# Performance work log

Measured on AMD Instinct MI355X. Metric: run time of the kernel, lower is better.

## Reference

```python
import jax, jax.numpy as jnp
import numpy as np

N = 20000   # nodes
E = 320000  # directed edges (before self-loops)
D = 64      # input_dim
H = 10      # GAT heads
HD = H * D  # 640
NEG_SLOPE = 0.2


def setup_inputs() -> dict:
    key = jax.random.key(0)
    ks = jax.random.split(key, 10)
    return {
        "x": jax.random.normal(ks[0], (N, D), jnp.float32),
        "W_gat": jax.random.normal(ks[1], (D, HD), jnp.float32) / np.sqrt(D).astype(np.float32),
        "att_src": jax.random.normal(ks[2], (H, D), jnp.float32) / np.sqrt(D).astype(np.float32),
        "att_dst": jax.random.normal(ks[3], (H, D), jnp.float32) / np.sqrt(D).astype(np.float32),
        "b_gat": jnp.zeros((HD,), jnp.float32),
        "W_gcn": jax.random.normal(ks[4], (HD, HD), jnp.float32) / np.sqrt(HD).astype(np.float32),
        "b_gcn": jnp.zeros((HD,), jnp.float32),
        "W1": jax.random.normal(ks[5], (2 * HD, 1500), jnp.float32) / np.sqrt(2 * HD).astype(np.float32),
        "b1": jnp.zeros((1500,), jnp.float32),
        "W2": jax.random.normal(ks[6], (1500, 10), jnp.float32) / np.sqrt(1500).astype(np.float32),
        "b2": jnp.zeros((10,), jnp.float32),
        "edge_index": jax.random.randint(ks[7], (2, E), 0, N, dtype=jnp.int64),
    }


def _forward(x, W_gat, att_src, att_dst, b_gat, W_gcn, b_gcn, W1, b1, W2, b2, edge_index):
    n = x.shape[0]
    # add self-loops (PyG default for both GATConv and GCNConv)
    loop = jnp.arange(n, dtype=edge_index.dtype)
    ei = jnp.concatenate([edge_index, jnp.stack([loop, loop])], axis=1)
    src, dst = ei[0], ei[1]

    # ---- GATConv(D -> D, heads=H, concat) ----
    xl = (x @ W_gat).reshape(n, H, D)                      # [N,H,D]
    a_src = jnp.einsum('nhd,hd->nh', xl, att_src)          # [N,H]
    a_dst = jnp.einsum('nhd,hd->nh', xl, att_dst)          # [N,H]
    alpha = jax.nn.leaky_relu(a_src[src] + a_dst[dst], NEG_SLOPE)  # [E',H]
    m = jax.ops.segment_max(alpha, dst, num_segments=n)    # segment softmax over incoming edges
    ex = jnp.exp(alpha - m[dst])
    den = jax.ops.segment_sum(ex, dst, num_segments=n)
    w = ex / (den[dst] + 1e-16)                            # [E',H]
    msg = xl[src] * w[:, :, None]                          # [E',H,D]
    x1 = jax.ops.segment_sum(msg, dst, num_segments=n).reshape(n, HD) + b_gat
    x1 = jax.nn.relu(x1)

    # ---- GCNConv(HD -> HD), symmetric norm with self-loops ----
    deg = jax.ops.segment_sum(jnp.ones(ei.shape[1], x.dtype), dst, num_segments=n)
    dinv = jnp.where(deg > 0, jax.lax.rsqrt(deg), 0.0)
    norm = dinv[src] * dinv[dst]                           # [E']
    xw = x1 @ W_gcn                                        # [N,HD]
    x2 = jax.ops.segment_sum(xw[src] * norm[:, None], dst, num_segments=n) + b_gcn
    x2 = jax.nn.relu(x2)

    # ---- global max/mean pool (batch=None -> single graph) + MLP head ----
    pooled = jnp.concatenate([x2.max(axis=0, keepdims=True),
                              x2.mean(axis=0, keepdims=True)], axis=1)  # [1, 2*HD]
    h = jax.nn.relu(pooled @ W1 + b1)
    # dropout is identity in eval mode
    return h @ W2 + b2                                     # [1, 10]


def reference(x, W_gat, att_src, att_dst, b_gat, W_gcn, b_gcn, W1, b1, W2, b2, edge_index):
    return _forward(x, W_gat, att_src, att_dst, b_gat, W_gcn, b_gcn, W1, b1, W2, b2, edge_index)
```

## Files before the change

kernel.cpp:

```cpp
#include <hip/hip_runtime.h>
#include <hip/hip_bf16.h>
#include <math.h>

#define NN 20000
#define DD 64
#define HH 10
#define HDIM 640
#define NEG 0.2f
#define H1 1500
#define ASTRIDE 12
#define BKK 128

typedef _Float16 half8 __attribute__((ext_vector_type(8)));
typedef _Float16 half4v __attribute__((ext_vector_type(4)));
typedef float f32x4 __attribute__((ext_vector_type(4)));

__global__ __launch_bounds__(256) void k_cvtB(const float* __restrict__ Wgcn,
                                              const float* __restrict__ Wg,
                                              _Float16* __restrict__ Wbt,
                                              _Float16* __restrict__ WgT)
{
    __shared__ float t[32][33];
    const int bx = blockIdx.x;
    int by = blockIdx.y;
    const float* W; _Float16* WT; int rows, cols;
    if (by < 20) { W = Wgcn; WT = Wbt; rows = HDIM; cols = HDIM; }
    else         { W = Wg;   WT = WgT; rows = DD;   cols = HDIM; by -= 20; }
    const int lx = threadIdx.x & 31, ly = threadIdx.x >> 5;
    #pragma unroll
    for (int i = ly; i < 32; i += 8)
        t[i][lx] = W[(size_t)(by * 32 + i) * cols + bx * 32 + lx];
    __syncthreads();
    #pragma unroll
    for (int j = ly; j < 32; j += 8)
        WT[(size_t)(bx * 32 + j) * rows + by * 32 + lx] = (_Float16)t[lx][j];
}

__global__ __launch_bounds__(256) void k_gemm1(
    const float* __restrict__ x, const _Float16* __restrict__ WgT,
    const float* __restrict__ att_s, const float* __restrict__ att_d,
    _Float16* __restrict__ xl, float* __restrict__ a_src, float* __restrict__ a_dst)
{
    __shared__ _Float16 As[128][72];
    __shared__ _Float16 Bs[64][72];
    const int tid = threadIdx.x;
    const int m0 = blockIdx.x * 128;
    const int h  = blockIdx.y;
    const int n0 = h * 64;

    {
        const int row = tid >> 1, ch = (tid & 1) * 32;
        const int gr = m0 + row;
        if (gr < NN) {
            const float* xp = &x[(size_t)gr * DD + ch];
            #pragma unroll
            for (int i = 0; i < 8; ++i) {
                const float4 v = *(const float4*)&xp[i * 4];
                half4v o = {(_Float16)v.x, (_Float16)v.y, (_Float16)v.z, (_Float16)v.w};
                *(half4v*)&As[row][ch + i * 4] = o;
            }
        } else {
            const half8 z = {0, 0, 0, 0, 0, 0, 0, 0};
            #pragma unroll
            for (int i = 0; i < 4; ++i) *(half8*)&As[row][ch + i * 8] = z;
        }
    }
    {
        const int row = tid >> 2, part = (tid & 3) * 16;
        const _Float16* wp = &WgT[(size_t)(n0 + row) * DD + part];
        *(half8*)&Bs[row][part]     = *(const half8*)&wp[0];
        *(half8*)&Bs[row][part + 8] = *(const half8*)&wp[8];
    }
    __syncthreads();

    const int lane = tid & 63, wave = tid >> 6;
    const int l15 = lane & 15, quad = lane >> 4;
    f32x4 acc[2][4];
    #pragma unroll
    for (int r = 0; r < 2; ++r)
        #pragma unroll
        for (int c = 0; c < 4; ++c) acc[r][c] = (f32x4){0.f, 0.f, 0.f, 0.f};

    #pragma unroll
    for (int ks = 0; ks < 2; ++ks) {
        const half8 a0 = *(const half8*)&As[wave * 32 + l15][ks * 32 + quad * 8];
        const half8 a1 = *(const half8*)&As[wave * 32 + 16 + l15][ks * 32 + quad * 8];
        #pragma unroll
        for (int c = 0; c < 4; ++c) {
            const half8 b = *(const half8*)&Bs[c * 16 + l15][ks * 32 + quad * 8];
            acc[0][c] = __builtin_amdgcn_mfma_f32_16x16x32_f16(a0, b, acc[0][c], 0, 0, 0);
            acc[1][c] = __builtin_amdgcn_mfma_f32_16x16x32_f16(a1, b, acc[1][c], 0, 0, 0);
        }
    }

    float asv[4], adv[4];
    #pragma unroll
    for (int c = 0; c < 4; ++c) {
        asv[c] = att_s[h * DD + c * 16 + l15];
        adv[c] = att_d[h * DD + c * 16 + l15];
    }
    #pragma unroll
    for (int r = 0; r < 2; ++r) {
        float ps[4] = {0.f, 0.f, 0.f, 0.f}, pd[4] = {0.f, 0.f, 0.f, 0.f};
        #pragma unroll
        for (int c = 0; c < 4; ++c)
            #pragma unroll
            for (int g = 0; g < 4; ++g) {
                ps[g] = fmaf(acc[r][c][g], asv[c], ps[g]);
                pd[g] = fmaf(acc[r][c][g], adv[c], pd[g]);
            }
        #pragma unroll
        for (int m = 1; m <= 8; m <<= 1)
            #pragma unroll
            for (int g = 0; g < 4; ++g) {
                ps[g] += __shfl_xor(ps[g], m);
                pd[g] += __shfl_xor(pd[g], m);
            }
        #pragma unroll
        for (int c = 0; c < 4; ++c)
            #pragma unroll
            for (int g = 0; g < 4; ++g) {
                const int row = m0 + wave * 32 + r * 16 + quad * 4 + g;
                if (row < NN)
                    xl[(size_t)row * HDIM + n0 + c * 16 + l15] = (_Float16)acc[r][c][g];
            }
        if (l15 == 0)
            #pragma unroll
            for (int g = 0; g < 4; ++g) {
                const int row = m0 + wave * 32 + r * 16 + quad * 4 + g;
                if (row < NN) {
                    a_src[(size_t)row * ASTRIDE + h] = ps[g];
                    a_dst[(size_t)row * ASTRIDE + h] = pd[g];
                }
            }
    }
}

__global__ void k_count(const int* __restrict__ ei, int E, int* __restrict__ cnt)
{
    const int e = blockIdx.x * blockDim.x + threadIdx.x;
    if (e >= E + NN) return;
    const int d = (e < E) ? ei[E + e] : (e - E);
    atomicAdd(&cnt[d], 1);
}

__global__ __launch_bounds__(1024) void k_scan(const int* __restrict__ cnt,
                                               int* __restrict__ rowptr,
                                               float* __restrict__ dinv)
{
    __shared__ int sh[1024];
    const int t = threadIdx.x;
    const int CH = 20;
    const int base = t * CH;
    int loc[CH];
    int s = 0;
    #pragma unroll
    for (int i = 0; i < CH; ++i) {
        const int idx = base + i;
        const int c = (idx < NN) ? cnt[idx] : 0;
        loc[i] = s; s += c;
    }
    sh[t] = s; __syncthreads();
    for (int off = 1; off < 1024; off <<= 1) {
        const int v = (t >= off) ? sh[t - off] : 0;
        __syncthreads();
        sh[t] += v;
        __syncthreads();
    }
    const int prev = (t == 0) ? 0 : sh[t - 1];
    #pragma unroll
    for (int i = 0; i < CH; ++i) {
        const int idx = base + i;
        if (idx < NN) {
            rowptr[idx] = prev + loc[i];
            dinv[idx]   = rsqrtf((float)cnt[idx]);
        }
    }
    if (t == 1023) rowptr[NN] = sh[1023];
}

__global__ void k_fill(const int* __restrict__ ei, int E,
                       const int* __restrict__ rowptr,
                       int* __restrict__ cursor, int* __restrict__ csr,
                       const float* __restrict__ dinv, float* __restrict__ wn,
                       const float* __restrict__ aS, const float* __restrict__ aD,
                       float* __restrict__ wgatT)
{
    const int EP = E + NN;
    const int e = blockIdx.x * blockDim.x + threadIdx.x;
    if (e >= EP) return;
    int s, d;
    if (e < E) { s = ei[e]; d = ei[E + e]; } else { s = d = e - E; }
    const int pos = atomicAdd(&cursor[d], 1);
    const int idx = rowptr[d] + pos;
    csr[idx] = s;
    wn[idx]  = dinv[s] * dinv[d];

    const f32x4 s0 = *(const f32x4*)&aS[(size_t)s * ASTRIDE];
    const f32x4 s1 = *(const f32x4*)&aS[(size_t)s * ASTRIDE + 4];
    const float2 s2 = *(const float2*)&aS[(size_t)s * ASTRIDE + 8];
    const f32x4 d0 = *(const f32x4*)&aD[(size_t)d * ASTRIDE];
    const f32x4 d1 = *(const f32x4*)&aD[(size_t)d * ASTRIDE + 4];
    const float2 d2 = *(const float2*)&aD[(size_t)d * ASTRIDE + 8];
    const float av[10] = {s0.x + d0.x, s0.y + d0.y, s0.z + d0.z, s0.w + d0.w,
                          s1.x + d1.x, s1.y + d1.y, s1.z + d1.z, s1.w + d1.w,
                          s2.x + d2.x, s2.y + d2.y};
    #pragma unroll
    for (int h = 0; h < 10; ++h) {
        float a = av[h];
        a = (a >= 0.f) ? a : NEG * a;
        wgatT[(size_t)h * EP + idx] = __expf(a);
    }
}

__device__ __forceinline__ bool slice_map3(int bid, int& s, int& m)
{
    const int r = bid & 7, k = bid >> 3;
    if (k < 625) { s = r; m = k; return true; }
    s = 8 + (r >> 2);
    m = (r & 3) * 157 + (k - 625);
    return m < 625;
}

__global__ __launch_bounds__(256) void k_gat_gather3(
    const int* __restrict__ rowptr, const int* __restrict__ csr,
    const float* __restrict__ wgatT, const _Float16* __restrict__ xl,
    const float* __restrict__ b_gat, _Float16* __restrict__ x1, int EP)
{
    int s, m;
    if (!slice_map3(blockIdx.x, s, m)) return;
    const int wave = threadIdx.x >> 6, lane = threadIdx.x & 63;
    const int g = lane >> 3, l = lane & 7;
    const int n = m * 32 + wave * 8 + g;
    const int col = s * 64 + l * 8;
    const float* __restrict__ wp = wgatT + (size_t)s * EP;
    const _Float16* __restrict__ xc = xl + col;

    float acc[8];
    #pragma unroll
    for (int i = 0; i < 8; ++i) acc[i] = 0.f;
    float ws = 0.f;

    const int j0 = rowptr[n], j1 = rowptr[n + 1];
    int j = j0;
    for (; j + 3 < j1; j += 4) {
        const int sA = csr[j], sB = csr[j + 1], sC = csr[j + 2], sD = csr[j + 3];
        const float wA = wp[j], wB = wp[j + 1], wC = wp[j + 2], wD = wp[j + 3];
        ws += wA + wB + wC + wD;
        const half8 vA = *(const half8*)&xc[(size_t)sA * HDIM];
        const half8 vB = *(const half8*)&xc[(size_t)sB * HDIM];
        const half8 vC = *(const half8*)&xc[(size_t)sC * HDIM];
        const half8 vD = *(const half8*)&xc[(size_t)sD * HDIM];
        #pragma unroll
        for (int i = 0; i < 8; ++i) {
            acc[i] = fmaf(wA, (float)vA[i], acc[i]);
            acc[i] = fmaf(wB, (float)vB[i], acc[i]);
            acc[i] = fmaf(wC, (float)vC[i], acc[i]);
            acc[i] = fmaf(wD, (float)vD[i], acc[i]);
        }
    }
    for (; j < j1; ++j) {
        const int sA = csr[j];
        const float wA = wp[j];
        ws += wA;
        const half8 vA = *(const half8*)&xc[(size_t)sA * HDIM];
        #pragma unroll
        for (int i = 0; i < 8; ++i) acc[i] = fmaf(wA, (float)vA[i], acc[i]);
    }

    const float rr = 1.f / (ws + 1e-16f);
    const float4 ba = *(const float4*)&b_gat[col];
    const float4 bb = *(const float4*)&b_gat[col + 4];
    const float bv[8] = {ba.x, ba.y, ba.z, ba.w, bb.x, bb.y, bb.z, bb.w};
    half8 o;
    #pragma unroll
    for (int i = 0; i < 8; ++i) {
        const float v = fmaf(acc[i], rr, bv[i]);
        o[i] = (_Float16)((v > 0.f) ? v : 0.f);
    }
    *(half8*)&x1[(size_t)n * HDIM + col] = o;
}

__global__ __launch_bounds__(256) void k_gcn_gather3(
    const int* __restrict__ rowptr, const int* __restrict__ csr,
    const float* __restrict__ wn, const _Float16* __restrict__ x1,
    _Float16* __restrict__ t)
{
    int s, m;
    if (!slice_map3(blockIdx.x, s, m)) return;
    const int wave = threadIdx.x >> 6, lane = threadIdx.x & 63;
    const int g = lane >> 3, l = lane & 7;
    const int n = m * 32 + wave * 8 + g;
    const int col = s * 64 + l * 8;
    const _Float16* __restrict__ xc = x1 + col;

    float acc[8];
    #pragma unroll
    for (int i = 0; i < 8; ++i) acc[i] = 0.f;

    const int j0 = rowptr[n], j1 = rowptr[n + 1];
    int j = j0;
    for (; j + 3 < j1; j += 4) {
        const int sA = csr[j], sB = csr[j + 1], sC = csr[j + 2], sD = csr[j + 3];
        const float wA = wn[j], wB = wn[j + 1], wC = wn[j + 2], wD = wn[j + 3];
        const half8 vA = *(const half8*)&xc[(size_t)sA * HDIM];
        const half8 vB = *(const half8*)&xc[(size_t)sB * HDIM];
        const half8 vC = *(const half8*)&xc[(size_t)sC * HDIM];
        const half8 vD = *(const half8*)&xc[(size_t)sD * HDIM];
        #pragma unroll
        for (int i = 0; i < 8; ++i) {
            acc[i] = fmaf(wA, (float)vA[i], acc[i]);
            acc[i] = fmaf(wB, (float)vB[i], acc[i]);
            acc[i] = fmaf(wC, (float)vC[i], acc[i]);
            acc[i] = fmaf(wD, (float)vD[i], acc[i]);
        }
    }
    for (; j < j1; ++j) {
        const int sA = csr[j];
        const float wA = wn[j];
        const half8 vA = *(const half8*)&xc[(size_t)sA * HDIM];
        #pragma unroll
        for (int i = 0; i < 8; ++i) acc[i] = fmaf(wA, (float)vA[i], acc[i]);
    }

    half8 o;
    #pragma unroll
    for (int i = 0; i < 8; ++i) o[i] = (_Float16)acc[i];
    *(half8*)&t[(size_t)n * HDIM + col] = o;
}

__global__ __launch_bounds__(256) void k_gemm2(const _Float16* __restrict__ X,
                                               const _Float16* __restrict__ Wbt,
                                               const float* __restrict__ b_gcn,
                                               float* __restrict__ pmax,
                                               float* __restrict__ psum)
{
    __shared__ _Float16 Bs[128 * BKK];
    const int tid = threadIdx.x;
    const int lane = tid & 63, wave = tid >> 6;
    const int l15 = lane & 15, quad = lane >> 4;
    const int m0 = blockIdx.x * 128 + wave * 32;
    const int n0 = blockIdx.y * 128;
    const int l7 = l15 & 7;

    f32x4 acc[2][8];
    #pragma unroll
    for (int r = 0; r < 2; ++r)
        #pragma unroll
        for (int c = 0; c < 8; ++c) acc[r][c] = (f32x4){0.f, 0.f, 0.f, 0.f};

    const int jrow = lane >> 4;
    const int jchunk = lane & 15;

    const _Float16* a0p = &X[(size_t)(m0 + l15) * HDIM + quad * 8];
    const _Float16* a1p = a0p + (size_t)16 * HDIM;

    for (int kb = 0; kb < HDIM; kb += BKK) {
        #pragma unroll
        for (int i = 0; i < 8; ++i) {
            const int r = (wave * 8 + i) * 4 + jrow;
            const int ck = jchunk ^ (r & 7);
            const _Float16* src = &Wbt[(size_t)(n0 + r) * HDIM + kb + ck * 8];
            __builtin_amdgcn_global_load_lds(
                (const __attribute__((address_space(1))) void*)src,
                (__attribute__((address_space(3))) void*)&Bs[(size_t)(wave * 8 + i) * 512],
                16, 0, 0);
        }
        half8 a0[4], a1[4];
        #pragma unroll
        for (int ks = 0; ks < 4; ++ks) {
            a0[ks] = *(const half8*)(a0p + kb + ks * 32);
            a1[ks] = *(const half8*)(a1p + kb + ks * 32);
        }
        __syncthreads();
        #pragma unroll
        for (int ks = 0; ks < 4; ++ks) {
            #pragma unroll
            for (int c = 0; c < 8; ++c) {
                const int br = c * 16 + l15;
                const int ck = (4 * ks + quad) ^ l7;
                const half8 b = *(const half8*)&Bs[(size_t)br * BKK + ck * 8];
                acc[0][c] = __builtin_amdgcn_mfma_f32_16x16x32_f16(a0[ks], b, acc[0][c], 0, 0, 0);
                acc[1][c] = __builtin_amdgcn_mfma_f32_16x16x32_f16(a1[ks], b, acc[1][c], 0, 0, 0);
            }
        }
        __syncthreads();
    }

    float lmax[8], lsum[8];
    #pragma unroll
    for (int c = 0; c < 8; ++c) { lmax[c] = 0.f; lsum[c] = 0.f; }
    #pragma unroll
    for (int c = 0; c < 8; ++c) {
        const float bb = b_gcn[n0 + c * 16 + l15];
        #pragma unroll
        for (int r = 0; r < 2; ++r)
            #pragma unroll
            for (int g = 0; g < 4; ++g) {
                const int row = m0 + r * 16 + quad * 4 + g;
                if (row < NN) {
                    float v = acc[r][c][g] + bb;
                    v = (v > 0.f) ? v : 0.f;
                    lmax[c] = fmaxf(lmax[c], v);
                    lsum[c] += v;
                }
            }
    }
    float* redm = (float*)Bs;
    float* reds = redm + 128;
    if (tid < 128) { redm[tid] = 0.f; reds[tid] = 0.f; }
    __syncthreads();
    #pragma unroll
    for (int c = 0; c < 8; ++c) {
        const int col = c * 16 + l15;
        atomicMax((int*)&redm[col], __float_as_int(lmax[c]));
        atomicAdd(&reds[col], lsum[c]);
    }
    __syncthreads();
    if (tid < 128) {
        atomicMax((int*)&pmax[n0 + tid], __float_as_int(redm[tid]));
        atomicAdd(&psum[n0 + tid], reds[tid]);
    }
}

__global__ __launch_bounds__(256) void k_mlp1(const float* __restrict__ pmax,
                                              const float* __restrict__ psum,
                                              const float* __restrict__ W1,
                                              float* __restrict__ hacc)
{
    __shared__ float pl[80];
    const int t = threadIdx.x;
    const int i0 = blockIdx.y * 80;
    if (t < 80) {
        const int i = i0 + t;
        pl[t] = (i < HDIM) ? pmax[i] : psum[i - HDIM] * (1.0f / NN);
    }
    __syncthreads();
    const int j = blockIdx.x * 256 + t;
    if (j >= H1) return;
    float acc = 0.f;
    #pragma unroll 8
    for (int i = 0; i < 80; ++i)
        acc = fmaf(pl[i], W1[(size_t)(i0 + i) * H1 + j], acc);
    atomicAdd(&hacc[j], acc);
}

__global__ __launch_bounds__(256) void k_mlp2(const float* __restrict__ hacc,
                                              const float* __restrict__ b1,
                                              const float* __restrict__ W2,
                                              const float* __restrict__ b2,
                                              float* __restrict__ out)
{
    __shared__ float hsh[H1];
    __shared__ float red[256];
    const int t = threadIdx.x;
    for (int i = t; i < H1; i += 256) {
        const float v = hacc[i] + b1[i];
        hsh[i] = (v > 0.f) ? v : 0.f;
    }
    __syncthreads();
    float acc[10];
    #pragma unroll
    for (int k = 0; k < 10; ++k) acc[k] = 0.f;
    for (int i = t; i < H1; i += 256) {
        const float h = hsh[i];
        #pragma unroll
        for (int k = 0; k < 10; ++k) acc[k] = fmaf(h, W2[i * 10 + k], acc[k]);
    }
    for (int k = 0; k < 10; ++k) {
        red[t] = acc[k]; __syncthreads();
        for (int s2 = 128; s2 > 0; s2 >>= 1) {
            if (t < s2) red[t] += red[t + s2];
            __syncthreads();
        }
        if (t == 0) out[k] = red[0] + b2[k];
        __syncthreads();
    }
}

extern "C" void kernel_launch(void* const* d_in, const int* in_sizes, int n_in,
                              void* d_out, int out_size, void* d_ws, size_t ws_size,
                              hipStream_t stream)
{
    const float* x     = (const float*)d_in[0];
    const float* Wg    = (const float*)d_in[1];
    const float* att_s = (const float*)d_in[2];
    const float* att_d = (const float*)d_in[3];
    const float* b_gat = (const float*)d_in[4];
    const float* Wgcn  = (const float*)d_in[5];
    const float* b_gcn = (const float*)d_in[6];
    const float* W1    = (const float*)d_in[7];
    const float* b1    = (const float*)d_in[8];
    const float* W2    = (const float*)d_in[9];
    const float* b2    = (const float*)d_in[10];
    const int*   ei    = (const int*)d_in[11];
    const int E = in_sizes[11] / 2;
    const int EP = E + NN;
    float* out = (float*)d_out;

    char* wsp = (char*)d_ws;
    size_t off = 0;
    auto alc = [&](size_t b) { void* p = wsp + off; off += (b + 255) & ~(size_t)255; return p; };
    _Float16* bufA = (_Float16*)alc((size_t)NN * HDIM * 2);
    _Float16* bufB = (_Float16*)alc((size_t)NN * HDIM * 2);
    float* aS     = (float*)alc((size_t)NN * ASTRIDE * 4);
    float* aD     = (float*)alc((size_t)NN * ASTRIDE * 4);
    int*   rowptr = (int*)alc((size_t)(NN + 1) * 4);
    int*   csr    = (int*)alc((size_t)EP * 4);
    float* dinv   = (float*)alc((size_t)NN * 4);
    float* wn     = (float*)alc((size_t)EP * 4);
    float* wgatT  = (float*)alc((size_t)EP * HH * 4);
    _Float16* Wbt = (_Float16*)alc((size_t)HDIM * HDIM * 2);
    _Float16* WgT = (_Float16*)alc((size_t)HDIM * DD * 2);
    const size_t zoff = off;
    int*   cnt    = (int*)alc((size_t)NN * 4);
    int*   cursor = (int*)alc((size_t)NN * 4);
    float* pmax   = (float*)alc((size_t)HDIM * 4);
    float* psum   = (float*)alc((size_t)HDIM * 4);
    float* hacc   = (float*)alc((size_t)H1 * 4);
    const size_t zsize = off - zoff;

    hipMemsetAsync(cnt, 0, zsize, stream);

    dim3 gw(HDIM / 32, HDIM / 32 + DD / 32);
    k_cvtB<<<gw, 256, 0, stream>>>(Wgcn, Wg, Wbt, WgT);
    dim3 g1((NN + 127) / 128, HH);
    k_gemm1<<<g1, 256, 0, stream>>>(x, WgT, att_s, att_d, bufA, aS, aD);
    k_count<<<(EP + 255) / 256, 256, 0, stream>>>(ei, E, cnt);
    k_scan<<<1, 1024, 0, stream>>>(cnt, rowptr, dinv);
    k_fill<<<(EP + 255) / 256, 256, 0, stream>>>(ei, E, rowptr, cursor, csr,
                                                 dinv, wn, aS, aD, wgatT);
    const int GG = 6256;
    k_gat_gather3<<<GG, 256, 0, stream>>>(rowptr, csr, wgatT, bufA, b_gat, bufB, EP);
    k_gcn_gather3<<<GG, 256, 0, stream>>>(rowptr, csr, wn, bufB, bufA);
    dim3 g2((NN + 127) / 128, HDIM / 128);
    k_gemm2<<<g2, 256, 0, stream>>>(bufA, Wbt, b_gcn, pmax, psum);
    dim3 gm1(6, 16);
    k_mlp1<<<gm1, 256, 0, stream>>>(pmax, psum, W1, hacc);
    k_mlp2<<<1, 256, 0, stream>>>(hacc, b1, W2, b2, out);
}
```

Measured before the change: 361.7 us.

## Compute GAT and GCN edge weights on the fly in gather kernels

```diff
diff --git a/kernel.cpp b/kernel.cpp
--- a/kernel.cpp
+++ b/kernel.cpp
@@ -8,7 +8,6 @@
 #define HDIM 640
 #define NEG 0.2f
 #define H1 1500
-#define ASTRIDE 12
 #define BKK 128
 
 typedef _Float16 half8 __attribute__((ext_vector_type(8)));
@@ -39,7 +38,7 @@
 __global__ __launch_bounds__(256) void k_gemm1(
     const float* __restrict__ x, const _Float16* __restrict__ WgT,
     const float* __restrict__ att_s, const float* __restrict__ att_d,
-    _Float16* __restrict__ xl, float* __restrict__ a_src, float* __restrict__ a_dst)
+    _Float16* __restrict__ xl, float* __restrict__ aST, float* __restrict__ aDT)
 {
     __shared__ _Float16 As[128][72];
     __shared__ _Float16 Bs[64][72];
@@ -129,8 +128,8 @@
             for (int g = 0; g < 4; ++g) {
                 const int row = m0 + wave * 32 + r * 16 + quad * 4 + g;
                 if (row < NN) {
-                    a_src[(size_t)row * ASTRIDE + h] = ps[g];
-                    a_dst[(size_t)row * ASTRIDE + h] = pd[g];
+                    aST[(size_t)h * NN + row] = ps[g];
+                    aDT[(size_t)h * NN + row] = pd[g];
                 }
             }
     }
@@ -181,36 +180,14 @@
 
 __global__ void k_fill(const int* __restrict__ ei, int E,
                        const int* __restrict__ rowptr,
-                       int* __restrict__ cursor, int* __restrict__ csr,
-                       const float* __restrict__ dinv, float* __restrict__ wn,
-                       const float* __restrict__ aS, const float* __restrict__ aD,
-                       float* __restrict__ wgatT)
-{
-    const int EP = E + NN;
+                       int* __restrict__ cursor, int* __restrict__ csr)
+{
     const int e = blockIdx.x * blockDim.x + threadIdx.x;
-    if (e >= EP) return;
+    if (e >= E + NN) return;
     int s, d;
     if (e < E) { s = ei[e]; d = ei[E + e]; } else { s = d = e - E; }
     const int pos = atomicAdd(&cursor[d], 1);
-    const int idx = rowptr[d] + pos;
-    csr[idx] = s;
-    wn[idx]  = dinv[s] * dinv[d];
-
-    const f32x4 s0 = *(const f32x4*)&aS[(size_t)s * ASTRIDE];
-    const f32x4 s1 = *(const f32x4*)&aS[(size_t)s * ASTRIDE + 4];
-    const float2 s2 = *(const float2*)&aS[(size_t)s * ASTRIDE + 8];
-    const f32x4 d0 = *(const f32x4*)&aD[(size_t)d * ASTRIDE];
-    const f32x4 d1 = *(const f32x4*)&aD[(size_t)d * ASTRIDE + 4];
-    const float2 d2 = *(const float2*)&aD[(size_t)d * ASTRIDE + 8];
-    const float av[10] = {s0.x + d0.x, s0.y + d0.y, s0.z + d0.z, s0.w + d0.w,
-                          s1.x + d1.x, s1.y + d1.y, s1.z + d1.z, s1.w + d1.w,
-                          s2.x + d2.x, s2.y + d2.y};
-    #pragma unroll
-    for (int h = 0; h < 10; ++h) {
-        float a = av[h];
-        a = (a >= 0.f) ? a : NEG * a;
-        wgatT[(size_t)h * EP + idx] = __expf(a);
-    }
+    csr[rowptr[d] + pos] = s;
 }
 
 __device__ __forceinline__ bool slice_map3(int bid, int& s, int& m)
@@ -222,10 +199,17 @@
     return m < 625;
 }
 
-__global__ __launch_bounds__(256) void k_gat_gather3(
+__device__ __forceinline__ float lrexp(float a)
+{
+    a = (a >= 0.f) ? a : NEG * a;
+    return __expf(a);
+}
+
+__global__ __launch_bounds__(256) void k_gat_gather4(
     const int* __restrict__ rowptr, const int* __restrict__ csr,
-    const float* __restrict__ wgatT, const _Float16* __restrict__ xl,
-    const float* __restrict__ b_gat, _Float16* __restrict__ x1, int EP)
+    const float* __restrict__ aST, const float* __restrict__ aDT,
+    const _Float16* __restrict__ xl, const float* __restrict__ b_gat,
+    _Float16* __restrict__ x1)
 {
     int s, m;
     if (!slice_map3(blockIdx.x, s, m)) return;
@@ -233,8 +217,9 @@
     const int g = lane >> 3, l = lane & 7;
     const int n = m * 32 + wave * 8 + g;
     const int col = s * 64 + l * 8;
-    const float* __restrict__ wp = wgatT + (size_t)s * EP;
+    const float* __restrict__ as = aST + (size_t)s * NN;
     const _Float16* __restrict__ xc = xl + col;
+    const float ad = aDT[(size_t)s * NN + n];
 
     float acc[8];
     #pragma unroll
@@ -245,7 +230,10 @@
     int j = j0;
     for (; j + 3 < j1; j += 4) {
         const int sA = csr[j], sB = csr[j + 1], sC = csr[j + 2], sD = csr[j + 3];
-        const float wA = wp[j], wB = wp[j + 1], wC = wp[j + 2], wD = wp[j + 3];
+        const float wA = lrexp(as[sA] + ad);
+        const float wB = lrexp(as[sB] + ad);
+        const float wC = lrexp(as[sC] + ad);
+        const float wD = lrexp(as[sD] + ad);
         ws += wA + wB + wC + wD;
         const half8 vA = *(const half8*)&xc[(size_t)sA * HDIM];
         const half8 vB = *(const half8*)&xc[(size_t)sB * HDIM];
@@ -261,7 +249,7 @@
     }
     for (; j < j1; ++j) {
         const int sA = csr[j];
-        const float wA = wp[j];
+        const float wA = lrexp(as[sA] + ad);
         ws += wA;
         const half8 vA = *(const half8*)&xc[(size_t)sA * HDIM];
         #pragma unroll
@@ -281,9 +269,9 @@
     *(half8*)&x1[(size_t)n * HDIM + col] = o;
 }
 
-__global__ __launch_bounds__(256) void k_gcn_gather3(
+__global__ __launch_bounds__(256) void k_gcn_gather4(
     const int* __restrict__ rowptr, const int* __restrict__ csr,
-    const float* __restrict__ wn, const _Float16* __restrict__ x1,
+    const float* __restrict__ dinv, const _Float16* __restrict__ x1,
     _Float16* __restrict__ t)
 {
     int s, m;
@@ -293,6 +281,7 @@
     const int n = m * 32 + wave * 8 + g;
     const int col = s * 64 + l * 8;
     const _Float16* __restrict__ xc = x1 + col;
+    const float dd = dinv[n];
 
     float acc[8];
     #pragma unroll
@@ -302,7 +291,8 @@
     int j = j0;
     for (; j + 3 < j1; j += 4) {
         const int sA = csr[j], sB = csr[j + 1], sC = csr[j + 2], sD = csr[j + 3];
-        const float wA = wn[j], wB = wn[j + 1], wC = wn[j + 2], wD = wn[j + 3];
+        const float wA = dinv[sA] * dd, wB = dinv[sB] * dd;
+        const float wC = dinv[sC] * dd, wD = dinv[sD] * dd;
         const half8 vA = *(const half8*)&xc[(size_t)sA * HDIM];
         const half8 vB = *(const half8*)&xc[(size_t)sB * HDIM];
         const half8 vC = *(const half8*)&xc[(size_t)sC * HDIM];
@@ -317,7 +307,7 @@
     }
     for (; j < j1; ++j) {
         const int sA = csr[j];
-        const float wA = wn[j];
+        const float wA = dinv[sA] * dd;
         const half8 vA = *(const half8*)&xc[(size_t)sA * HDIM];
         #pragma unroll
         for (int i = 0; i < 8; ++i) acc[i] = fmaf(wA, (float)vA[i], acc[i]);
@@ -503,13 +493,11 @@
     auto alc = [&](size_t b) { void* p = wsp + off; off += (b + 255) & ~(size_t)255; return p; };
     _Float16* bufA = (_Float16*)alc((size_t)NN * HDIM * 2);
     _Float16* bufB = (_Float16*)alc((size_t)NN * HDIM * 2);
-    float* aS     = (float*)alc((size_t)NN * ASTRIDE * 4);
-    float* aD     = (float*)alc((size_t)NN * ASTRIDE * 4);
+    float* aST    = (float*)alc((size_t)HH * NN * 4);
+    float* aDT    = (float*)alc((size_t)HH * NN * 4);
     int*   rowptr = (int*)alc((size_t)(NN + 1) * 4);
     int*   csr    = (int*)alc((size_t)EP * 4);
     float* dinv   = (float*)alc((size_t)NN * 4);
-    float* wn     = (float*)alc((size_t)EP * 4);
-    float* wgatT  = (float*)alc((size_t)EP * HH * 4);
     _Float16* Wbt = (_Float16*)alc((size_t)HDIM * HDIM * 2);
     _Float16* WgT = (_Float16*)alc((size_t)HDIM * DD * 2);
     const size_t zoff = off;
@@ -525,14 +513,13 @@
     dim3 gw(HDIM / 32, HDIM / 32 + DD / 32);
     k_cvtB<<<gw, 256, 0, stream>>>(Wgcn, Wg, Wbt, WgT);
     dim3 g1((NN + 127) / 128, HH);
-    k_gemm1<<<g1, 256, 0, stream>>>(x, WgT, att_s, att_d, bufA, aS, aD);
+    k_gemm1<<<g1, 256, 0, stream>>>(x, WgT, att_s, att_d, bufA, aST, aDT);
     k_count<<<(EP + 255) / 256, 256, 0, stream>>>(ei, E, cnt);
     k_scan<<<1, 1024, 0, stream>>>(cnt, rowptr, dinv);
-    k_fill<<<(EP + 255) / 256, 256, 0, stream>>>(ei, E, rowptr, cursor, csr,
-                                                 dinv, wn, aS, aD, wgatT);
+    k_fill<<<(EP + 255) / 256, 256, 0, stream>>>(ei, E, rowptr, cursor, csr);
     const int GG = 6256;
-    k_gat_gather3<<<GG, 256, 0, stream>>>(rowptr, csr, wgatT, bufA, b_gat, bufB, EP);
-    k_gcn_gather3<<<GG, 256, 0, stream>>>(rowptr, csr, wn, bufB, bufA);
+    k_gat_gather4<<<GG, 256, 0, stream>>>(rowptr, csr, aST, aDT, bufA, b_gat, bufB);
+    k_gcn_gather4<<<GG, 256, 0, stream>>>(rowptr, csr, dinv, bufB, bufA);
     dim3 g2((NN + 127) / 128, HDIM / 128);
     k_gemm2<<<g2, 256, 0, stream>>>(bufA, Wbt, b_gcn, pmax, psum);
     dim3 gm1(6, 16);
```

New measurement: 324.8 us. -10.2%, faster.
